# Performance work log

Measured on AMD Instinct MI355X. Metric: run time of the kernel, lower is better.

## Reference

```python
import jax, jax.numpy as jnp
import numpy as np

B, S, D, H = 4, 2048, 512, 8
DEPTH = D // H
BAND = 16  # log_thresholds [1,2,4,8,16] union == distance <= 16


def setup_inputs() -> dict:
    key = jax.random.key(0)
    ks = jax.random.split(key, 11)
    sc = 0.02
    return {
        "q": jax.random.normal(ks[0], (B, S, D), jnp.float32),
        "k": jax.random.normal(ks[1], (B, S, D), jnp.float32),
        "v": jax.random.normal(ks[2], (B, S, D), jnp.float32),
        "wq": jax.random.normal(ks[3], (D, D), jnp.float32) * sc,
        "bq": jnp.zeros((D,), jnp.float32),
        "wk": jax.random.normal(ks[4], (D, D), jnp.float32) * sc,
        "bk": jnp.zeros((D,), jnp.float32),
        "wv": jax.random.normal(ks[5], (D, D), jnp.float32) * sc,
        "bv": jnp.zeros((D,), jnp.float32),
        "wo": jax.random.normal(ks[6], (D, D), jnp.float32) * sc,
        "bo": jnp.zeros((D,), jnp.float32),
    }


def _split_heads(x):
    # [B,S,D] -> [B,H,S,depth]
    b, s, _ = x.shape
    return x.reshape(b, s, H, DEPTH).transpose(0, 2, 1, 3)


def reference(q, k, v, wq, bq, wk, bk, wv, bv, wo, bo):
    qh = _split_heads(q @ wq + bq)
    kh = _split_heads(k @ wk + bk)
    vh = _split_heads(v @ wv + bv)
    scale = 1.0 / jnp.sqrt(jnp.float32(DEPTH))
    logits = jnp.einsum("bhqd,bhkd->bhqk", qh, kh) * scale  # [B,H,S,S]
    idx = jnp.arange(S)
    keep = jnp.abs(idx[:, None] - idx[None, :]) <= BAND  # band mask [S,S]
    logits = jnp.where(keep[None, None], logits, jnp.float32(-1e9))
    attn = jax.nn.softmax(logits, axis=-1)
    out = jnp.einsum("bhqk,bhkd->bhqd", attn, vh)
    out = out.transpose(0, 2, 1, 3).reshape(q.shape[0], -1, D)
    return out @ wo + bo
```

## Files before the change

kernel.cpp:

```cpp
#include <hip/hip_runtime.h>

typedef unsigned int uint;
typedef unsigned short ushort;
typedef __attribute__((ext_vector_type(8))) short bf16x8;
typedef __attribute__((ext_vector_type(4))) float f32x4;

namespace {
constexpr int kS = 2048;
constexpr int kD = 512;
constexpr int kH = 8;
constexpr int kBand = 16;

constexpr size_t kQpk = 0;
constexpr size_t kKpk = 4194304;
constexpr size_t kVpk = kKpk + 4259840;
constexpr size_t kObp = kVpk + 4259840;
constexpr size_t kApk = kObp + 4194304;
constexpr size_t kBpk = kApk + 12582912;
}

static __device__ __forceinline__ ushort f2bf(float f) {
  uint u = __builtin_bit_cast(uint, f);
  u = (u + 0x7fffu + ((u >> 16) & 1u)) >> 16;
  return (ushort)u;
}

static __device__ __forceinline__ bf16x8 cvt8(f32x4 lo, f32x4 hi) {
  uint4 r;
  asm("v_cvt_pk_bf16_f32 %0, %1, %2" : "=v"(r.x) : "v"(lo[0]), "v"(lo[1]));
  asm("v_cvt_pk_bf16_f32 %0, %1, %2" : "=v"(r.y) : "v"(lo[2]), "v"(lo[3]));
  asm("v_cvt_pk_bf16_f32 %0, %1, %2" : "=v"(r.z) : "v"(hi[0]), "v"(hi[1]));
  asm("v_cvt_pk_bf16_f32 %0, %1, %2" : "=v"(r.w) : "v"(hi[2]), "v"(hi[3]));
  return __builtin_bit_cast(bf16x8, r);
}


__global__ __launch_bounds__(256) void prep_all(
    const float* __restrict__ q, const float* __restrict__ k,
    const float* __restrict__ v, const float* __restrict__ wq,
    const float* __restrict__ wk, const float* __restrict__ wv,
    const float* __restrict__ wo, ushort* __restrict__ ws) {
  __shared__ float Ws[64][65];
  const int blk = blockIdx.x, tid = threadIdx.x;
  if (blk < 384) {
    const int z = blk >> 7, rb = blk & 127;
    const float* X = z == 0 ? q : (z == 1 ? k : v);
    ushort* A = ws + kApk + (size_t)z * 4194304 + (size_t)rb * 32768;
    const int tl = tid >> 2, dq = tid & 3;
    const float* src = X + (size_t)(rb * 64 + tl) * kD + dq * 8;
    ushort* dstb = A + (tl >> 4) * 512 + (dq * 16 + (tl & 15)) * 8;
#pragma unroll
    for (int c = 0; c < 16; ++c) {
      const f32x4 lo = *(const f32x4*)(src + c * 32);
      const f32x4 hi = *(const f32x4*)(src + c * 32 + 4);
      *(bf16x8*)(dstb + c * 2048) = cvt8(lo, hi);
    }
    return;
  }
  if (blk >= 640) {
    const int idx = blk - 640;
    const int bh = idx >> 1, gg = (idx & 1) * 64;
    ushort* p = ws + kVpk + ((size_t)(bh * 65 + gg) * 4) * 512 + tid * 8;
    *(uint4*)p = (uint4){0, 0, 0, 0};
    return;
  }
  const int w = blk - 384;
  const int z = w >> 6;
  const float* W = z == 0 ? wq : (z == 1 ? wk : (z == 2 ? wv : wo));
  const int kt = ((w >> 3) & 7) * 64, nt = (w & 7) * 64;
  const int r = tid >> 2, c0 = (tid & 3) * 16;
#pragma unroll
  for (int i = 0; i < 4; ++i) {
    const float4 x =
        *(const float4*)(W + (size_t)(kt + r) * kD + nt + c0 + i * 4);
    Ws[r][c0 + i * 4 + 0] = x.x;
    Ws[r][c0 + i * 4 + 1] = x.y;
    Ws[r][c0 + i * 4 + 2] = x.z;
    Ws[r][c0 + i * 4 + 3] = x.w;
  }
  __syncthreads();
  const int nl = tid >> 2, k0 = (tid & 3) * 16;
  alignas(16) ushort tmp[16];
#pragma unroll
  for (int i = 0; i < 16; ++i) tmp[i] = f2bf(Ws[k0 + i][nl]);
  const int ng = nt + nl, kg = kt + k0;
  const int c = ng >> 6, sub = (ng >> 4) & 3, l = ng & 15;
  const int it = kg >> 5, q0 = (kg >> 3) & 3;
  ushort* base = ws + kBpk + ((size_t)(z * 8 + c) * 16 + it) * 2048 +
                 (sub * 64 + l) * 8;
  *(uint4*)(base + q0 * 128) = *(const uint4*)&tmp[0];
  *(uint4*)(base + (q0 + 1) * 128) = *(const uint4*)&tmp[8];
}

__global__ __launch_bounds__(64) void gemm_qkv(
    const ushort* __restrict__ ws_c, ushort* __restrict__ ws,
    const float* __restrict__ bq, const float* __restrict__ bk,
    const float* __restrict__ bv) {
  __shared__ alignas(16) ushort Tl[64 * 72];

  const int lane = threadIdx.x, l15 = lane & 15, qd = lane >> 4;
  const int lin = blockIdx.x;
  const int xcd = lin & 7, j = lin >> 3;
  const int ct = j & 7;
  const int rtl = xcd + 8 * (j >> 3);
  const int mode = rtl >> 7, rt = rtl & 127;
  const int row0 = rt * 64;

  const float* bias = mode == 0 ? bq : (mode == 1 ? bk : bv);
  const ushort* pa =
      ws_c + kApk + (size_t)mode * 4194304 + (size_t)rt * 32768 + lane * 8;
  const ushort* pb =
      ws_c + kBpk + ((size_t)(mode * 8 + ct) * 16) * 2048 + lane * 8;

  f32x4 acc[4][4];
#pragma unroll
  for (int mi = 0; mi < 4; ++mi)
#pragma unroll
    for (int ni = 0; ni < 4; ++ni) acc[mi][ni] = (f32x4)(0.f);

  bf16x8 Af[3][4], Bf[3][4];
#define LDSET(s, itv)                                                  \
  {                                                                    \
    _Pragma("unroll") for (int x = 0; x < 4; ++x) {                    \
      Af[s][x] = *(const bf16x8*)(pa + (itv)*2048 + x * 512);          \
      Bf[s][x] = *(const bf16x8*)(pb + (itv)*2048 + x * 512);          \
    }                                                                  \
  }
  LDSET(0, 0);
  LDSET(1, 1);
#pragma unroll
  for (int it = 0; it < 16; ++it) {
    if (it < 14) LDSET((it + 2) % 3, it + 2);
    const int s = it % 3;
#pragma unroll
    for (int mi = 0; mi < 4; ++mi)
#pragma unroll
      for (int ni = 0; ni < 4; ++ni)
        acc[mi][ni] = __builtin_amdgcn_mfma_f32_16x16x32_bf16(
            Af[s][mi], Bf[s][ni], acc[mi][ni], 0, 0, 0);
  }
#undef LDSET

  float bcol[4];
#pragma unroll
  for (int ni = 0; ni < 4; ++ni) bcol[ni] = bias[ct * 64 + ni * 16 + l15];

  const int bh = (row0 >> 11) * kH + ct;
  if (mode <= 1) {
#pragma unroll
    for (int mi = 0; mi < 4; ++mi)
#pragma unroll
      for (int ni = 0; ni < 4; ++ni)
#pragma unroll
        for (int r = 0; r < 4; ++r)
          Tl[(mi * 16 + qd * 4 + r) * 72 + ni * 16 + l15] =
              f2bf(acc[mi][ni][r] + bcol[ni]);
    asm volatile("s_waitcnt lgkmcnt(0)" ::: "memory");
    const int s = (row0 & (kS - 1)) + lane;
    const int g = s >> 4;
    const ushort* Trow = &Tl[lane * 72];
    ushort* base =
        (mode == 0)
            ? ws + kQpk + ((size_t)(bh * 128 + g) * 2) * 512 + (s & 15) * 8
            : ws + kKpk + ((size_t)(bh * 130 + g + 1) * 2) * 512 + (s & 15) * 8;
#pragma unroll
    for (int cc = 0; cc < 8; ++cc)
      *(uint4*)(base + (cc >> 2) * 512 + (cc & 3) * 128) =
          *(const uint4*)&Trow[cc * 8];
  } else {
#pragma unroll
    for (int mi = 0; mi < 4; ++mi)
#pragma unroll
      for (int ni = 0; ni < 4; ++ni)
#pragma unroll
        for (int r = 0; r < 4; ++r)
          Tl[(ni * 16 + l15) * 72 + mi * 16 + qd * 4 + r] =
              f2bf(acc[mi][ni][r] + bcol[ni]);
    asm volatile("s_waitcnt lgkmcnt(0)" ::: "memory");
    const int nt = lane >> 4, l15v = lane & 15;
    const int sb = (row0 & (kS - 1)) + 16;
    const ushort* Trow = &Tl[lane * 72];
#pragma unroll
    for (int cc = 0; cc < 8; ++cc) {
      const int sc = sb + cc * 8;
      const int gg = sc >> 5, khc = (sc >> 3) & 3;
      ushort* dst = ws + kVpk + ((size_t)(bh * 65 + gg) * 4 + nt) * 512 +
                    khc * 128 + l15v * 8;
      *(uint4*)dst = *(const uint4*)&Trow[cc * 8];
    }
  }
}

__global__ __launch_bounds__(64, 2) void attn_kernel(
    const ushort* __restrict__ ws_c, ushort* __restrict__ ws) {
  __shared__ alignas(16) ushort Pl[32 * 72];

  const int lane = threadIdx.x, l15 = lane & 15, qd = lane >> 4;
  const int bh = blockIdx.y;
  const int q0 = blockIdx.x * 32;
  const ushort* Qpk = ws_c + kQpk;
  const ushort* Kpk = ws_c + kKpk;
  const ushort* Vpk = ws_c + kVpk;

  bf16x8 qf[2][2], kf[4][2];
#pragma unroll
  for (int mi = 0; mi < 2; ++mi)
#pragma unroll
    for (int kc = 0; kc < 2; ++kc)
      qf[mi][kc] = *(const bf16x8*)&Qpk[((size_t)(bh * 128 + (q0 >> 4) + mi) *
                                            2 + kc) * 512 + lane * 8];
#pragma unroll
  for (int ni = 0; ni < 4; ++ni)
#pragma unroll
    for (int kc = 0; kc < 2; ++kc)
      kf[ni][kc] = *(const bf16x8*)&Kpk[((size_t)(bh * 130 + (q0 >> 4) + ni) *
                                            2 + kc) * 512 + lane * 8];

  f32x4 S[2][4];
#pragma unroll
  for (int mi = 0; mi < 2; ++mi)
#pragma unroll
    for (int ni = 0; ni < 4; ++ni) S[mi][ni] = (f32x4)(0.f);
#pragma unroll
  for (int mi = 0; mi < 2; ++mi)
#pragma unroll
    for (int ni = 0; ni < 4; ++ni)
#pragma unroll
      for (int kc = 0; kc < 2; ++kc)
        S[mi][ni] = __builtin_amdgcn_mfma_f32_16x16x32_bf16(
            qf[mi][kc], kf[ni][kc], S[mi][ni], 0, 0, 0);

#pragma unroll
  for (int mi = 0; mi < 2; ++mi)
#pragma unroll
    for (int ni = 0; ni < 4; ++ni)
#pragma unroll
      for (int r = 0; r < 4; ++r) {
        const int q_local = mi * 16 + qd * 4 + r;
        const int key_local = ni * 16 + l15;
        const int key = q0 - kBand + key_local;
        const int dlt = key_local - q_local;
        const bool ok = (dlt >= 0) && (dlt <= 32) && (key >= 0) && (key < kS);
        S[mi][ni][r] = ok ? S[mi][ni][r] * 0.125f : -3.0e38f;
      }

  float inv[2][4];
#pragma unroll
  for (int mi = 0; mi < 2; ++mi)
#pragma unroll
    for (int r = 0; r < 4; ++r) {
      float m = S[mi][0][r];
#pragma unroll
      for (int ni = 1; ni < 4; ++ni) m = fmaxf(m, S[mi][ni][r]);
      m = fmaxf(m, __shfl_xor(m, 1));
      m = fmaxf(m, __shfl_xor(m, 2));
      m = fmaxf(m, __shfl_xor(m, 4));
      m = fmaxf(m, __shfl_xor(m, 8));
      float s = 0.f;
#pragma unroll
      for (int ni = 0; ni < 4; ++ni) {
        const float e = __expf(S[mi][ni][r] - m);
        S[mi][ni][r] = e;
        s += e;
      }
      s += __shfl_xor(s, 1);
      s += __shfl_xor(s, 2);
      s += __shfl_xor(s, 4);
      s += __shfl_xor(s, 8);
      inv[mi][r] = 1.f / s;
    }

#pragma unroll
  for (int mi = 0; mi < 2; ++mi)
#pragma unroll
    for (int ni = 0; ni < 4; ++ni)
#pragma unroll
      for (int r = 0; r < 4; ++r)
        Pl[(mi * 16 + qd * 4 + r) * 72 + ni * 16 + l15] = f2bf(S[mi][ni][r]);
  __syncthreads();

  f32x4 O[2][4];
#pragma unroll
  for (int mi = 0; mi < 2; ++mi)
#pragma unroll
    for (int nt = 0; nt < 4; ++nt) O[mi][nt] = (f32x4)(0.f);

#pragma unroll
  for (int kc = 0; kc < 2; ++kc) {
    bf16x8 pf[2], vfr[4];
#pragma unroll
    for (int mi = 0; mi < 2; ++mi)
      pf[mi] = *(const bf16x8*)&Pl[(mi * 16 + l15) * 72 + kc * 32 + qd * 8];
#pragma unroll
    for (int nt = 0; nt < 4; ++nt)
      vfr[nt] = *(const bf16x8*)&Vpk[((size_t)(bh * 65 + (q0 >> 5) + kc) * 4 +
                                       nt) * 512 + lane * 8];
#pragma unroll
    for (int mi = 0; mi < 2; ++mi)
#pragma unroll
      for (int nt = 0; nt < 4; ++nt)
        O[mi][nt] = __builtin_amdgcn_mfma_f32_16x16x32_bf16(pf[mi], vfr[nt],
                                                            O[mi][nt], 0, 0, 0);
  }

#pragma unroll
  for (int mi = 0; mi < 2; ++mi)
#pragma unroll
    for (int nt = 0; nt < 4; ++nt)
#pragma unroll
      for (int r = 0; r < 4; ++r)
        Pl[(mi * 16 + qd * 4 + r) * 72 + nt * 16 + l15] =
            f2bf(O[mi][nt][r] * inv[mi][r]);
  asm volatile("s_waitcnt lgkmcnt(0)" ::: "memory");

  const int row = lane >> 1, half = lane & 1;
  const int tglob = (bh >> 3) * kS + q0 + row;
  const int rt = tglob >> 6, mi2 = (tglob >> 4) & 3, l15o = tglob & 15;
  const int h = bh & 7;
  ushort* Obp = ws + kObp;
#pragma unroll
  for (int jj = 0; jj < 4; ++jj) {
    const int cc = half * 4 + jj;
    const int it2 = h * 2 + (cc >> 2), qd2 = cc & 3;
    ushort* dst = Obp + ((size_t)(rt * 16 + it2) * 4 + mi2) * 512 +
                  (qd2 * 16 + l15o) * 8;
    *(uint4*)dst = *(const uint4*)&Pl[row * 72 + cc * 8];
  }
}

__global__ __launch_bounds__(64) void gemm_out(
    const ushort* __restrict__ ws_c, const float* __restrict__ bo,
    float* __restrict__ outp) {
  const int lane = threadIdx.x, l15 = lane & 15, qd = lane >> 4;
  const int lin = blockIdx.x;
  const int xcd = lin & 7, j = lin >> 3;
  const int ct = j & 7;
  const int rt = xcd + 8 * (j >> 3);
  const int row0 = rt * 64;

  const ushort* pa = ws_c + kObp + (size_t)rt * 32768 + lane * 8;
  const ushort* pb =
      ws_c + kBpk + ((size_t)(3 * 8 + ct) * 16) * 2048 + lane * 8;

  f32x4 acc[4][4];
#pragma unroll
  for (int mi = 0; mi < 4; ++mi)
#pragma unroll
    for (int ni = 0; ni < 4; ++ni) acc[mi][ni] = (f32x4)(0.f);

  bf16x8 Af[3][4], Bf[3][4];
#define LDSET(s, itv)                                                  \
  {                                                                    \
    _Pragma("unroll") for (int x = 0; x < 4; ++x) {                    \
      Af[s][x] = *(const bf16x8*)(pa + (itv)*2048 + x * 512);          \
      Bf[s][x] = *(const bf16x8*)(pb + (itv)*2048 + x * 512);          \
    }                                                                  \
  }
  LDSET(0, 0);
  LDSET(1, 1);
#pragma unroll
  for (int it = 0; it < 16; ++it) {
    if (it < 14) LDSET((it + 2) % 3, it + 2);
    const int s = it % 3;
#pragma unroll
    for (int mi = 0; mi < 4; ++mi)
#pragma unroll
      for (int ni = 0; ni < 4; ++ni)
        acc[mi][ni] = __builtin_amdgcn_mfma_f32_16x16x32_bf16(
            Af[s][mi], Bf[s][ni], acc[mi][ni], 0, 0, 0);
  }
#undef LDSET

#pragma unroll
  for (int ni = 0; ni < 4; ++ni) {
    const int colg = ct * 64 + ni * 16 + l15;
    const float bc = bo[colg];
#pragma unroll
    for (int mi = 0; mi < 4; ++mi)
#pragma unroll
      for (int r = 0; r < 4; ++r) {
        const int token = row0 + mi * 16 + qd * 4 + r;
        outp[(size_t)token * kD + colg] = acc[mi][ni][r] + bc;
      }
  }
}

extern "C" void kernel_launch(void* const* d_in, const int* in_sizes, int n_in,
                              void* d_out, int out_size, void* d_ws,
                              size_t ws_size, hipStream_t stream) {
  const float* q = (const float*)d_in[0];
  const float* k = (const float*)d_in[1];
  const float* v = (const float*)d_in[2];
  const float* wq = (const float*)d_in[3];
  const float* bq = (const float*)d_in[4];
  const float* wk = (const float*)d_in[5];
  const float* bk = (const float*)d_in[6];
  const float* wv = (const float*)d_in[7];
  const float* bv = (const float*)d_in[8];
  const float* wo = (const float*)d_in[9];
  const float* bo = (const float*)d_in[10];
  float* out = (float*)d_out;

  ushort* ws = (ushort*)d_ws;

  prep_all<<<dim3(704), 256, 0, stream>>>(q, k, v, wq, wk, wv, wo, ws);
  gemm_qkv<<<dim3(3072), 64, 0, stream>>>(ws, ws, bq, bk, bv);
  attn_kernel<<<dim3(kS / 32, 32), 64, 0, stream>>>(ws, ws);
  gemm_out<<<dim3(1024), 64, 0, stream>>>(ws, bo, out);
}
```

Measured before the change: 155.3 us.

## Fuse banded attention with output projection in one 8-wave block

Merges attn_kernel and gemm_out into a single kernel where each 512-thread block processes 32 query rows for all 8 heads of one batch, one wave per head. Each wave keeps its normalized attention output in shared memory, then after a block barrier every wave computes a 64-column slice of the output projection, reading A fragments from LDS. This removes the bf16 Obp round trip through global memory and one kernel launch. In exchange the grid shrinks to 256 blocks of 512 threads, and the Wo tiles are re-read by every block with less reuse per block, which may lower occupancy and projection efficiency.

```diff
diff --git a/kernel.cpp b/kernel.cpp
--- a/kernel.cpp
+++ b/kernel.cpp
@@ -33,7 +33,6 @@
   asm("v_cvt_pk_bf16_f32 %0, %1, %2" : "=v"(r.w) : "v"(hi[2]), "v"(hi[3]));
   return __builtin_bit_cast(bf16x8, r);
 }
-
 
 __global__ __launch_bounds__(256) void prep_all(
     const float* __restrict__ q, const float* __restrict__ k,
@@ -191,13 +190,18 @@
   }
 }
 
-__global__ __launch_bounds__(64, 2) void attn_kernel(
-    const ushort* __restrict__ ws_c, ushort* __restrict__ ws) {
-  __shared__ alignas(16) ushort Pl[32 * 72];
-
-  const int lane = threadIdx.x, l15 = lane & 15, qd = lane >> 4;
-  const int bh = blockIdx.y;
+__global__ __launch_bounds__(512) void attn_out(
+    const ushort* __restrict__ ws_c, const float* __restrict__ bo,
+    float* __restrict__ outp) {
+  __shared__ alignas(16) ushort Pl[8 * 32 * 72];
+
+  const int tid = threadIdx.x;
+  const int w = tid >> 6, lane = tid & 63, l15 = lane & 15, qd = lane >> 4;
+  const int b = blockIdx.y;
   const int q0 = blockIdx.x * 32;
+  const int bh = b * kH + w;
+  ushort* Plw = &Pl[w * 2304];
+
   const ushort* Qpk = ws_c + kQpk;
   const ushort* Kpk = ws_c + kKpk;
   const ushort* Vpk = ws_c + kVpk;
@@ -276,8 +280,8 @@
     for (int ni = 0; ni < 4; ++ni)
 #pragma unroll
       for (int r = 0; r < 4; ++r)
-        Pl[(mi * 16 + qd * 4 + r) * 72 + ni * 16 + l15] = f2bf(S[mi][ni][r]);
-  __syncthreads();
+        Plw[(mi * 16 + qd * 4 + r) * 72 + ni * 16 + l15] = f2bf(S[mi][ni][r]);
+  asm volatile("s_waitcnt lgkmcnt(0)" ::: "memory");
 
   f32x4 O[2][4];
 #pragma unroll
@@ -290,7 +294,7 @@
     bf16x8 pf[2], vfr[4];
 #pragma unroll
     for (int mi = 0; mi < 2; ++mi)
-      pf[mi] = *(const bf16x8*)&Pl[(mi * 16 + l15) * 72 + kc * 32 + qd * 8];
+      pf[mi] = *(const bf16x8*)&Plw[(mi * 16 + l15) * 72 + kc * 32 + qd * 8];
 #pragma unroll
     for (int nt = 0; nt < 4; ++nt)
       vfr[nt] = *(const bf16x8*)&Vpk[((size_t)(bh * 65 + (q0 >> 5) + kc) * 4 +
@@ -309,77 +313,53 @@
     for (int nt = 0; nt < 4; ++nt)
 #pragma unroll
       for (int r = 0; r < 4; ++r)
-        Pl[(mi * 16 + qd * 4 + r) * 72 + nt * 16 + l15] =
+        Plw[(mi * 16 + qd * 4 + r) * 72 + nt * 16 + l15] =
             f2bf(O[mi][nt][r] * inv[mi][r]);
-  asm volatile("s_waitcnt lgkmcnt(0)" ::: "memory");
-
-  const int row = lane >> 1, half = lane & 1;
-  const int tglob = (bh >> 3) * kS + q0 + row;
-  const int rt = tglob >> 6, mi2 = (tglob >> 4) & 3, l15o = tglob & 15;
-  const int h = bh & 7;
-  ushort* Obp = ws + kObp;
-#pragma unroll
-  for (int jj = 0; jj < 4; ++jj) {
-    const int cc = half * 4 + jj;
-    const int it2 = h * 2 + (cc >> 2), qd2 = cc & 3;
-    ushort* dst = Obp + ((size_t)(rt * 16 + it2) * 4 + mi2) * 512 +
-                  (qd2 * 16 + l15o) * 8;
-    *(uint4*)dst = *(const uint4*)&Pl[row * 72 + cc * 8];
-  }
-}
-
-__global__ __launch_bounds__(64) void gemm_out(
-    const ushort* __restrict__ ws_c, const float* __restrict__ bo,
-    float* __restrict__ outp) {
-  const int lane = threadIdx.x, l15 = lane & 15, qd = lane >> 4;
-  const int lin = blockIdx.x;
-  const int xcd = lin & 7, j = lin >> 3;
-  const int ct = j & 7;
-  const int rt = xcd + 8 * (j >> 3);
-  const int row0 = rt * 64;
-
-  const ushort* pa = ws_c + kObp + (size_t)rt * 32768 + lane * 8;
+
+  __syncthreads();
+
   const ushort* pb =
-      ws_c + kBpk + ((size_t)(3 * 8 + ct) * 16) * 2048 + lane * 8;
-
-  f32x4 acc[4][4];
-#pragma unroll
-  for (int mi = 0; mi < 4; ++mi)
+      ws_c + kBpk + ((size_t)(3 * 8 + w) * 16) * 2048 + lane * 8;
+
+  f32x4 acc[2][4];
+#pragma unroll
+  for (int mi = 0; mi < 2; ++mi)
 #pragma unroll
     for (int ni = 0; ni < 4; ++ni) acc[mi][ni] = (f32x4)(0.f);
 
-  bf16x8 Af[3][4], Bf[3][4];
-#define LDSET(s, itv)                                                  \
-  {                                                                    \
-    _Pragma("unroll") for (int x = 0; x < 4; ++x) {                    \
-      Af[s][x] = *(const bf16x8*)(pa + (itv)*2048 + x * 512);          \
-      Bf[s][x] = *(const bf16x8*)(pb + (itv)*2048 + x * 512);          \
-    }                                                                  \
-  }
-  LDSET(0, 0);
-  LDSET(1, 1);
+  bf16x8 Bf[2][4];
+#pragma unroll
+  for (int x = 0; x < 4; ++x) Bf[0][x] = *(const bf16x8*)(pb + x * 512);
 #pragma unroll
   for (int it = 0; it < 16; ++it) {
-    if (it < 14) LDSET((it + 2) % 3, it + 2);
-    const int s = it % 3;
-#pragma unroll
-    for (int mi = 0; mi < 4; ++mi)
+    if (it < 15) {
+#pragma unroll
+      for (int x = 0; x < 4; ++x)
+        Bf[(it + 1) & 1][x] =
+            *(const bf16x8*)(pb + (size_t)(it + 1) * 2048 + x * 512);
+    }
+    bf16x8 af[2];
+#pragma unroll
+    for (int mi = 0; mi < 2; ++mi)
+      af[mi] = *(const bf16x8*)&Pl[(it >> 1) * 2304 + (mi * 16 + l15) * 72 +
+                                   (it & 1) * 32 + qd * 8];
+#pragma unroll
+    for (int mi = 0; mi < 2; ++mi)
 #pragma unroll
       for (int ni = 0; ni < 4; ++ni)
         acc[mi][ni] = __builtin_amdgcn_mfma_f32_16x16x32_bf16(
-            Af[s][mi], Bf[s][ni], acc[mi][ni], 0, 0, 0);
-  }
-#undef LDSET
+            af[mi], Bf[it & 1][ni], acc[mi][ni], 0, 0, 0);
+  }
 
 #pragma unroll
   for (int ni = 0; ni < 4; ++ni) {
-    const int colg = ct * 64 + ni * 16 + l15;
+    const int colg = w * 64 + ni * 16 + l15;
     const float bc = bo[colg];
 #pragma unroll
-    for (int mi = 0; mi < 4; ++mi)
+    for (int mi = 0; mi < 2; ++mi)
 #pragma unroll
       for (int r = 0; r < 4; ++r) {
-        const int token = row0 + mi * 16 + qd * 4 + r;
+        const int token = b * kS + q0 + mi * 16 + qd * 4 + r;
         outp[(size_t)token * kD + colg] = acc[mi][ni][r] + bc;
       }
   }
@@ -405,6 +385,5 @@
 
   prep_all<<<dim3(704), 256, 0, stream>>>(q, k, v, wq, wk, wv, wo, ws);
   gemm_qkv<<<dim3(3072), 64, 0, stream>>>(ws, ws, bq, bk, bv);
-  attn_kernel<<<dim3(kS / 32, 32), 64, 0, stream>>>(ws, ws);
-  gemm_out<<<dim3(1024), 64, 0, stream>>>(ws, bo, out);
-}
+  attn_out<<<dim3(kS / 32, 4), 512, 0, stream>>>(ws, bo, out);
+}
```

New measurement: 149.1 us. 4.0% less time.
